# Optimization experiments

Hardware: AMD Instinct MI355X
Metric: run time of the kernel (lower is better)

## Reference

```python
import jax, jax.numpy as jnp
import numpy as np

D = 1024
E = 8


def setup_inputs() -> dict:
    key = jax.random.key(0)
    ks = jax.random.split(key, 7)
    s = 1.0 / np.sqrt(D)
    x = jax.random.normal(ks[0], (4, 2048, D), dtype=jnp.float32)
    Wg = jax.random.uniform(ks[1], (D, E), minval=-s, maxval=s, dtype=jnp.float32)
    bg = jax.random.uniform(ks[2], (E,), minval=-s, maxval=s, dtype=jnp.float32)
    W1 = jax.random.uniform(ks[3], (E, D, D), minval=-s, maxval=s, dtype=jnp.float32)
    b1 = jax.random.uniform(ks[4], (E, D), minval=-s, maxval=s, dtype=jnp.float32)
    W2 = jax.random.uniform(ks[5], (E, D, D), minval=-s, maxval=s, dtype=jnp.float32)
    b2 = jax.random.uniform(ks[6], (E, D), minval=-s, maxval=s, dtype=jnp.float32)
    return {"x": x, "Wg": Wg, "bg": bg, "W1": W1, "b1": b1, "W2": W2, "b2": b2}


def reference(x, Wg, bg, W1, b1, W2, b2):
    N, T, d = x.shape
    x_flat = x.reshape(N * T, d)                                  # [NT, D]
    logits = x_flat @ Wg + bg                                     # [NT, E]
    probs = jax.nn.softmax(logits, axis=-1)
    assignments = jnp.argmax(probs, axis=-1)                      # [NT]
    # all-experts MLP (dense, as in the original module)
    h = jnp.einsum('nd,edh->neh', x_flat, W1) + b1[None]          # [NT, E, D]
    h = jax.nn.gelu(h, approximate=False)                         # torch GELU = exact erf
    eo = jnp.einsum('neh,ehd->ned', h, W2) + b2[None]             # [NT, E, D]
    selected = jnp.take_along_axis(eo, assignments[:, None, None], axis=1)[:, 0, :]  # [NT, D]
    w = jnp.take_along_axis(probs, assignments[:, None], axis=1)  # [NT, 1]
    out = (w * selected).reshape(N, T, d)
    return out
```

## Files before the change

kernel.cpp:

```cpp
#include <hip/hip_runtime.h>
#include <cstdint>

#define NT 8192
#define DD 1024
#define NE 8
#define BK 32
#define NKIT (DD / BK)
#define TM 128
#define MAXTILE 72
#define TPX (MAXTILE / 8)

typedef __attribute__((ext_vector_type(8))) _Float16 half8;
typedef __attribute__((ext_vector_type(4))) float f32x4;

__device__ __forceinline__ unsigned short f2h_bits(float f) {
  _Float16 h = (_Float16)f;
  return __builtin_bit_cast(unsigned short, h);
}

#define GLDS16(gp, lp) __builtin_amdgcn_global_load_lds( \
  (__attribute__((address_space(1))) void*)(uintptr_t)(gp), \
  (__attribute__((address_space(3))) void*)(uintptr_t)(lp), 16, 0, 0)

#define WAITCNT_VM4  0xF74
#define WAITCNT_VM0  0xF70

__global__ __launch_bounds__(256) void prep_kernel(
    const float* __restrict__ W1, const float* __restrict__ W2,
    _Float16* __restrict__ W1t, _Float16* __restrict__ W2t,
    const float* __restrict__ x, const float* __restrict__ Wg, const float* __restrict__ bg,
    int* __restrict__ assign, float* __restrict__ wgt, _Float16* __restrict__ xh) {
  __shared__ alignas(16) char smem[32768];
  const int bid = blockIdx.x;
  const int tid = threadIdx.x;
  if (bid < 4096) {
    float (*tile)[65] = (float (*)[65])smem;
    const int z = bid >> 8;
    const float* W = (z < 8 ? W1 : W2) + (size_t)(z & 7) * (DD * DD);
    _Float16* Wt   = (z < 8 ? W1t : W2t) + (size_t)(z & 7) * (DD * DD);
    const int k0 = (bid & 15) * 64, n0 = ((bid >> 4) & 15) * 64;
#pragma unroll
    for (int it = 0; it < 4; ++it) {
      int idx = it * 256 + tid;
      int r = idx >> 4;
      int q = idx & 15;
      float4 v = *(const float4*)(W + (size_t)(k0 + r) * DD + n0 + q * 4);
      tile[r][q * 4 + 0] = v.x; tile[r][q * 4 + 1] = v.y;
      tile[r][q * 4 + 2] = v.z; tile[r][q * 4 + 3] = v.w;
    }
    __syncthreads();
#pragma unroll
    for (int it = 0; it < 4; ++it) {
      int idx = it * 256 + tid;
      int n = idx >> 4;
      int q = idx & 15;
      ushort4 o;
      o.x = f2h_bits(tile[q * 4 + 0][n]);
      o.y = f2h_bits(tile[q * 4 + 1][n]);
      o.z = f2h_bits(tile[q * 4 + 2][n]);
      o.w = f2h_bits(tile[q * 4 + 3][n]);
      *(ushort4*)(Wt + (size_t)(n0 + n) * DD + k0 + q * 4) = o;
    }
  } else {
    float* WgL = (float*)smem;
    const int gb = bid - 4096;
#pragma unroll
    for (int it = 0; it < 8; ++it) {
      int idx = it * 256 + tid;
      float4 v = ((const float4*)Wg)[idx];
      int k = idx >> 1;
      int e0 = (idx & 1) * 4;
      WgL[(e0 + 0) * DD + k] = v.x;
      WgL[(e0 + 1) * DD + k] = v.y;
      WgL[(e0 + 2) * DD + k] = v.z;
      WgL[(e0 + 3) * DD + k] = v.w;
    }
    __syncthreads();
    const int lane = tid & 63, w = tid >> 6;
#pragma unroll
    for (int s = 0; s < 2; ++s) {
      const int t = gb * 8 + w * 2 + s;
      const float4* xr = (const float4*)(x + (size_t)t * DD);
      float4 xv[4];
#pragma unroll
      for (int c = 0; c < 4; ++c) xv[c] = xr[lane + 64 * c];
      ushort4* xo = (ushort4*)(xh + (size_t)t * DD);
#pragma unroll
      for (int c = 0; c < 4; ++c) {
        union { ushort4 u; _Float16 h[4]; } cv;
        cv.h[0] = (_Float16)xv[c].x; cv.h[1] = (_Float16)xv[c].y;
        cv.h[2] = (_Float16)xv[c].z; cv.h[3] = (_Float16)xv[c].w;
        xo[lane + 64 * c] = cv.u;
      }
      float p[NE];
#pragma unroll
      for (int e = 0; e < NE; ++e) {
        float acc = 0.f;
#pragma unroll
        for (int c = 0; c < 4; ++c) {
          float4 wv = *(const float4*)&WgL[e * DD + 4 * lane + 256 * c];
          acc += xv[c].x * wv.x + xv[c].y * wv.y + xv[c].z * wv.z + xv[c].w * wv.w;
        }
        p[e] = acc;
      }
#pragma unroll
      for (int e = 0; e < NE; ++e) {
        float v = p[e];
        for (int off = 32; off > 0; off >>= 1) v += __shfl_down(v, off, 64);
        p[e] = v;
      }
      if (lane == 0) {
        float l[NE];
#pragma unroll
        for (int e = 0; e < NE; ++e) l[e] = p[e] + bg[e];
        int a = 0; float best = l[0];
#pragma unroll
        for (int e = 1; e < NE; ++e) if (l[e] > best) { best = l[e]; a = e; }
        float sum = 0.f;
#pragma unroll
        for (int e = 0; e < NE; ++e) sum += expf(l[e] - best);
        assign[t] = a;
        wgt[t] = 1.0f / sum;
      }
    }
  }
}

__global__ __launch_bounds__(1024) void sort_kernel(
    const int* __restrict__ assign, int* __restrict__ rowtok, int* __restrict__ plan) {
  __shared__ int sc[NE * 1024];
  __shared__ int s_pref[NE + 1];
  const int tid = threadIdx.x;
  int a[8];
  int c[NE];
#pragma unroll
  for (int e = 0; e < NE; ++e) c[e] = 0;
#pragma unroll
  for (int j = 0; j < 8; ++j) { a[j] = assign[tid * 8 + j]; ++c[a[j]]; }
#pragma unroll
  for (int e = 0; e < NE; ++e) sc[e * 1024 + tid] = c[e];
  __syncthreads();
  for (int d = 1; d < 1024; d <<= 1) {
    int add[NE];
    if (tid >= d) {
#pragma unroll
      for (int e = 0; e < NE; ++e) add[e] = sc[e * 1024 + tid - d];
    }
    __syncthreads();
    if (tid >= d) {
#pragma unroll
      for (int e = 0; e < NE; ++e) sc[e * 1024 + tid] += add[e];
    }
    __syncthreads();
  }
  int tot[NE], incl[NE];
#pragma unroll
  for (int e = 0; e < NE; ++e) { tot[e] = sc[e * 1024 + 1023]; incl[e] = sc[e * 1024 + tid]; }
  int offs[NE];
  {
    int s = 0;
#pragma unroll
    for (int e = 0; e < NE; ++e) { offs[e] = s; s += tot[e]; }
  }
  int run[NE];
#pragma unroll
  for (int e = 0; e < NE; ++e) run[e] = offs[e] + incl[e] - c[e];
#pragma unroll
  for (int j = 0; j < 8; ++j) { int e = a[j]; rowtok[run[e]++] = tid * 8 + j; }
  if (tid == 0) {
    int s = 0;
    for (int e = 0; e < NE; ++e) { s_pref[e] = s; s += (tot[e] + TM - 1) / TM; }
    s_pref[NE] = s;
    plan[0] = s;
  }
  __syncthreads();
  const int nt = s_pref[NE];
  if (tid < nt) {
    int e = 0;
    while (tid >= s_pref[e + 1]) ++e;
    int t = tid - s_pref[e];
    plan[1 + tid] = e;
    plan[1 + MAXTILE + tid] = offs[e] + t * TM;
    plan[1 + 2 * MAXTILE + tid] = offs[e] + tot[e];
  }
}

template <int MODE>
__global__ __launch_bounds__(256, 3) void gemm_kernel(
    const _Float16* __restrict__ A,
    const _Float16* __restrict__ Wt,
    const float* __restrict__ bias,
    const int* __restrict__ plan,
    _Float16* __restrict__ Hout,
    float* __restrict__ Fout,
    const int* __restrict__ rowtok,
    const float* __restrict__ wgt) {
  const int wrk = blockIdx.x;
  const int g = wrk & 7;
  const int r = wrk >> 3;
  const int tile = g * TPX + (r >> 3);
  const int nb = r & 7;
  if (tile >= plan[0]) return;
  const int e = plan[1 + tile];
  const int m0 = plan[1 + MAXTILE + tile];
  const int seg_end = plan[1 + 2 * MAXTILE + tile];
  const int n0 = nb * 128;

  const int tid = threadIdx.x;
  const int lane = tid & 63;
  const int wv = tid >> 6;
  const int wm = wv >> 1;
  const int wq = wv & 1;
  const int quad = lane >> 4;
  const int r15 = lane & 15;

  __shared__ alignas(16) char lds[49152];

  const _Float16* We = Wt + (size_t)e * DD * DD;
  const _Float16* gAp[2];
  const _Float16* gBp[2];
  int ldsoA[2], ldsoB[2];
#pragma unroll
  for (int i = 0; i < 2; ++i) {
    int slot = i * 256 + tid;
    int row = slot >> 2;
    int c = (slot & 3) ^ ((row >> 1) & 3);
    int rg = m0 + row; if (rg > NT - 1) rg = NT - 1;
    int arow = (MODE == 0) ? rowtok[rg] : rg;
    gAp[i] = A + (size_t)arow * DD + c * 8;
    ldsoA[i] = slot * 16;
    gBp[i] = We + (size_t)(n0 + row) * DD + c * 8;
    ldsoB[i] = slot * 16;
  }

  int aoff[4], boff[4];
#pragma unroll
  for (int i = 0; i < 4; ++i) {
    int m = wm * 64 + i * 16 + r15;
    aoff[i] = m * 4 + (quad ^ ((m >> 1) & 3));
    int n = wq * 64 + i * 16 + r15;
    boff[i] = n * 4 + (quad ^ ((n >> 1) & 3));
  }

  f32x4 acc[4][4];
  f32x4 zero4 = {0.f, 0.f, 0.f, 0.f};
#pragma unroll
  for (int mi = 0; mi < 4; ++mi)
#pragma unroll
    for (int ni = 0; ni < 4; ++ni) acc[mi][ni] = zero4;

#define LDSBUF(B) (lds + (B) * 16384)
#define STAGE(KT, BUF) do {                                          \
    const int ko_ = (KT) * BK;                                       \
    char* lb_ = LDSBUF(BUF);                                         \
    GLDS16(gAp[0] + ko_, lb_ + ldsoA[0]);                            \
    GLDS16(gAp[1] + ko_, lb_ + ldsoA[1]);                            \
    GLDS16(gBp[0] + ko_, lb_ + 8192 + ldsoB[0]);                     \
    GLDS16(gBp[1] + ko_, lb_ + 8192 + ldsoB[1]);                     \
  } while (0)
#define COMPUTE(BUF) do {                                            \
    const half8* AsV = (const half8*)(LDSBUF(BUF));                  \
    const half8* BsV = (const half8*)(LDSBUF(BUF) + 8192);           \
    half8 a_[4], b_[4];                                              \
    _Pragma("unroll")                                                \
    for (int i = 0; i < 4; ++i) a_[i] = AsV[aoff[i]];                \
    _Pragma("unroll")                                                \
    for (int i = 0; i < 4; ++i) b_[i] = BsV[boff[i]];                \
    _Pragma("unroll")                                                \
    for (int mi = 0; mi < 4; ++mi)                                   \
      _Pragma("unroll")                                              \
      for (int ni = 0; ni < 4; ++ni)                                 \
        acc[mi][ni] = __builtin_amdgcn_mfma_f32_16x16x32_f16(a_[mi], b_[ni], acc[mi][ni], 0, 0, 0); \
  } while (0)

  STAGE(0, 0);
  STAGE(1, 1);

#pragma unroll 1
  for (int kt = 0; kt < NKIT - 2; kt += 3) {
    __builtin_amdgcn_s_waitcnt(WAITCNT_VM4);
    __builtin_amdgcn_s_barrier();
    __asm__ volatile("" ::: "memory");
    STAGE(kt + 2, 2);
    COMPUTE(0);
    __builtin_amdgcn_s_waitcnt(WAITCNT_VM4);
    __builtin_amdgcn_s_barrier();
    __asm__ volatile("" ::: "memory");
    STAGE(kt + 3, 0);
    COMPUTE(1);
    __builtin_amdgcn_s_waitcnt(WAITCNT_VM4);
    __builtin_amdgcn_s_barrier();
    __asm__ volatile("" ::: "memory");
    STAGE(kt + 4, 1);
    COMPUTE(2);
  }
  __builtin_amdgcn_s_waitcnt(WAITCNT_VM4);
  __builtin_amdgcn_s_barrier();
  __asm__ volatile("" ::: "memory");
  COMPUTE(0);
  __builtin_amdgcn_s_waitcnt(WAITCNT_VM0);
  __builtin_amdgcn_s_barrier();
  __asm__ volatile("" ::: "memory");
  COMPUTE(1);
#undef COMPUTE
#undef STAGE
#undef LDSBUF

  const float* bptr = bias + (size_t)e * DD;
#pragma unroll
  for (int mi = 0; mi < 4; ++mi) {
    int rowb = m0 + wm * 64 + mi * 16 + quad * 4;
#pragma unroll
    for (int rr = 0; rr < 4; ++rr) {
      int gpos = rowb + rr;
      if (gpos < seg_end) {
        if (MODE == 0) {
#pragma unroll
          for (int ni = 0; ni < 4; ++ni) {
            int n = n0 + wq * 64 + ni * 16 + r15;
            float val = acc[mi][ni][rr] + bptr[n];
            val = 0.5f * val * (1.0f + erff(val * 0.70710678118654752f));
            Hout[(size_t)gpos * DD + n] = (_Float16)val;
          }
        } else {
          int tok = rowtok[gpos];
          float wgl = wgt[tok];
          float* orow = Fout + (size_t)tok * DD;
#pragma unroll
          for (int ni = 0; ni < 4; ++ni) {
            int n = n0 + wq * 64 + ni * 16 + r15;
            orow[n] = (acc[mi][ni][rr] + bptr[n]) * wgl;
          }
        }
      }
    }
  }
}

extern "C" void kernel_launch(void* const* d_in, const int* in_sizes, int n_in,
                              void* d_out, int out_size, void* d_ws, size_t ws_size,
                              hipStream_t stream) {
  const float* x  = (const float*)d_in[0];
  const float* Wg = (const float*)d_in[1];
  const float* bg = (const float*)d_in[2];
  const float* W1 = (const float*)d_in[3];
  const float* b1 = (const float*)d_in[4];
  const float* W2 = (const float*)d_in[5];
  const float* b2 = (const float*)d_in[6];
  float* out = (float*)d_out;

  char* ws = (char*)d_ws;
  const size_t MB16 = (size_t)1 << 24;
  _Float16* W1t = (_Float16*)(ws + 0 * MB16);
  _Float16* W2t = (_Float16*)(ws + 1 * MB16);
  _Float16* xh  = (_Float16*)(ws + 2 * MB16);
  _Float16* H   = (_Float16*)(ws + 3 * MB16);
  int*   assign = (int*)(ws + 4 * MB16);
  int*   rowtok = assign + NT;
  float* wgt    = (float*)(rowtok + NT);
  int*   plan   = (int*)(wgt + NT);

  prep_kernel<<<4096 + NT / 8, 256, 0, stream>>>(W1, W2, W1t, W2t, x, Wg, bg, assign, wgt, xh);
  sort_kernel<<<1, 1024, 0, stream>>>(assign, rowtok, plan);
  gemm_kernel<0><<<MAXTILE * 8, 256, 0, stream>>>(xh, W1t, b1, plan, H, nullptr, rowtok, nullptr);
  gemm_kernel<1><<<MAXTILE * 8, 256, 0, stream>>>(H, W2t, b2, plan, nullptr, out, rowtok, wgt);
}
```

Measured before the change: 230.4 us.

## Double K tile to 64 and switch to double-buffered LDS pipeline

```diff
diff --git a/kernel.cpp b/kernel.cpp
--- a/kernel.cpp
+++ b/kernel.cpp
@@ -4,7 +4,7 @@
 #define NT 8192
 #define DD 1024
 #define NE 8
-#define BK 32
+#define BK 64
 #define NKIT (DD / BK)
 #define TM 128
 #define MAXTILE 72
@@ -22,7 +22,6 @@
   (__attribute__((address_space(1))) void*)(uintptr_t)(gp), \
   (__attribute__((address_space(3))) void*)(uintptr_t)(lp), 16, 0, 0)
 
-#define WAITCNT_VM4  0xF74
 #define WAITCNT_VM0  0xF70
 
 __global__ __launch_bounds__(256) void prep_kernel(
@@ -186,7 +185,7 @@
 }
 
 template <int MODE>
-__global__ __launch_bounds__(256, 3) void gemm_kernel(
+__global__ __launch_bounds__(256, 2) void gemm_kernel(
     const _Float16* __restrict__ A,
     const _Float16* __restrict__ Wt,
     const float* __restrict__ bias,
@@ -214,17 +213,17 @@
   const int quad = lane >> 4;
   const int r15 = lane & 15;
 
-  __shared__ alignas(16) char lds[49152];
+  __shared__ alignas(16) char lds[65536];
 
   const _Float16* We = Wt + (size_t)e * DD * DD;
-  const _Float16* gAp[2];
-  const _Float16* gBp[2];
-  int ldsoA[2], ldsoB[2];
-#pragma unroll
-  for (int i = 0; i < 2; ++i) {
+  const _Float16* gAp[4];
+  const _Float16* gBp[4];
+  int ldsoA[4], ldsoB[4];
+#pragma unroll
+  for (int i = 0; i < 4; ++i) {
     int slot = i * 256 + tid;
-    int row = slot >> 2;
-    int c = (slot & 3) ^ ((row >> 1) & 3);
+    int row = slot >> 3;
+    int c = (slot & 7) ^ (row & 7);
     int rg = m0 + row; if (rg > NT - 1) rg = NT - 1;
     int arow = (MODE == 0) ? rowtok[rg] : rg;
     gAp[i] = A + (size_t)arow * DD + c * 8;
@@ -233,13 +232,16 @@
     ldsoB[i] = slot * 16;
   }
 
-  int aoff[4], boff[4];
+  int aoff[4][2], boff[4][2];
 #pragma unroll
   for (int i = 0; i < 4; ++i) {
-    int m = wm * 64 + i * 16 + r15;
-    aoff[i] = m * 4 + (quad ^ ((m >> 1) & 3));
-    int n = wq * 64 + i * 16 + r15;
-    boff[i] = n * 4 + (quad ^ ((n >> 1) & 3));
+#pragma unroll
+    for (int q = 0; q < 2; ++q) {
+      int m = wm * 64 + i * 16 + r15;
+      aoff[i][q] = m * 8 + ((q * 4 + quad) ^ (r15 & 7));
+      int n = wq * 64 + i * 16 + r15;
+      boff[i][q] = n * 8 + ((q * 4 + quad) ^ (r15 & 7));
+    }
   }
 
   f32x4 acc[4][4];
@@ -249,59 +251,51 @@
 #pragma unroll
     for (int ni = 0; ni < 4; ++ni) acc[mi][ni] = zero4;
 
-#define LDSBUF(B) (lds + (B) * 16384)
+#define LDSBUF(B) (lds + (B) * 32768)
 #define STAGE(KT, BUF) do {                                          \
     const int ko_ = (KT) * BK;                                       \
     char* lb_ = LDSBUF(BUF);                                         \
     GLDS16(gAp[0] + ko_, lb_ + ldsoA[0]);                            \
     GLDS16(gAp[1] + ko_, lb_ + ldsoA[1]);                            \
-    GLDS16(gBp[0] + ko_, lb_ + 8192 + ldsoB[0]);                     \
-    GLDS16(gBp[1] + ko_, lb_ + 8192 + ldsoB[1]);                     \
+    GLDS16(gAp[2] + ko_, lb_ + ldsoA[2]);                            \
+    GLDS16(gAp[3] + ko_, lb_ + ldsoA[3]);                            \
+    GLDS16(gBp[0] + ko_, lb_ + 16384 + ldsoB[0]);                    \
+    GLDS16(gBp[1] + ko_, lb_ + 16384 + ldsoB[1]);                    \
+    GLDS16(gBp[2] + ko_, lb_ + 16384 + ldsoB[2]);                    \
+    GLDS16(gBp[3] + ko_, lb_ + 16384 + ldsoB[3]);                    \
   } while (0)
 #define COMPUTE(BUF) do {                                            \
     const half8* AsV = (const half8*)(LDSBUF(BUF));                  \
-    const half8* BsV = (const half8*)(LDSBUF(BUF) + 8192);           \
-    half8 a_[4], b_[4];                                              \
+    const half8* BsV = (const half8*)(LDSBUF(BUF) + 16384);          \
     _Pragma("unroll")                                                \
-    for (int i = 0; i < 4; ++i) a_[i] = AsV[aoff[i]];                \
-    _Pragma("unroll")                                                \
-    for (int i = 0; i < 4; ++i) b_[i] = BsV[boff[i]];                \
-    _Pragma("unroll")                                                \
-    for (int mi = 0; mi < 4; ++mi)                                   \
+    for (int q = 0; q < 2; ++q) {                                    \
+      half8 a_[4], b_[4];                                            \
       _Pragma("unroll")                                              \
-      for (int ni = 0; ni < 4; ++ni)                                 \
-        acc[mi][ni] = __builtin_amdgcn_mfma_f32_16x16x32_f16(a_[mi], b_[ni], acc[mi][ni], 0, 0, 0); \
+      for (int i = 0; i < 4; ++i) a_[i] = AsV[aoff[i][q]];           \
+      _Pragma("unroll")                                              \
+      for (int i = 0; i < 4; ++i) b_[i] = BsV[boff[i][q]];           \
+      _Pragma("unroll")                                              \
+      for (int mi = 0; mi < 4; ++mi)                                 \
+        _Pragma("unroll")                                            \
+        for (int ni = 0; ni < 4; ++ni)                               \
+          acc[mi][ni] = __builtin_amdgcn_mfma_f32_16x16x32_f16(a_[mi], b_[ni], acc[mi][ni], 0, 0, 0); \
+    }                                                                \
   } while (0)
 
   STAGE(0, 0);
-  STAGE(1, 1);
-
-#pragma unroll 1
-  for (int kt = 0; kt < NKIT - 2; kt += 3) {
-    __builtin_amdgcn_s_waitcnt(WAITCNT_VM4);
-    __builtin_amdgcn_s_barrier();
-    __asm__ volatile("" ::: "memory");
-    STAGE(kt + 2, 2);
-    COMPUTE(0);
-    __builtin_amdgcn_s_waitcnt(WAITCNT_VM4);
-    __builtin_amdgcn_s_barrier();
-    __asm__ volatile("" ::: "memory");
-    STAGE(kt + 3, 0);
-    COMPUTE(1);
-    __builtin_amdgcn_s_waitcnt(WAITCNT_VM4);
-    __builtin_amdgcn_s_barrier();
-    __asm__ volatile("" ::: "memory");
-    STAGE(kt + 4, 1);
-    COMPUTE(2);
-  }
-  __builtin_amdgcn_s_waitcnt(WAITCNT_VM4);
-  __builtin_amdgcn_s_barrier();
-  __asm__ volatile("" ::: "memory");
-  COMPUTE(0);
   __builtin_amdgcn_s_waitcnt(WAITCNT_VM0);
   __builtin_amdgcn_s_barrier();
   __asm__ volatile("" ::: "memory");
-  COMPUTE(1);
+
+#pragma unroll 1
+  for (int kt = 0; kt < NKIT; ++kt) {
+    const int buf = kt & 1;
+    if (kt + 1 < NKIT) STAGE(kt + 1, buf ^ 1);
+    COMPUTE(buf);
+    __builtin_amdgcn_s_waitcnt(WAITCNT_VM0);
+    __builtin_amdgcn_s_barrier();
+    __asm__ volatile("" ::: "memory");
+  }
 #undef COMPUTE
 #undef STAGE
 #undef LDSBUF
```

New measurement: 244.5 us. +6.1%, slower.
